# Performance work log

Measured on AMD Instinct MI355X. Metric: run time of the kernel, lower is better.

Reference implementation:

```python
import jax, jax.numpy as jnp
import numpy as np

NUM_USERS = 100000
NUM_ITEMS = 50000
NUM_HIDDEN = 64
NUM_BINS = 10
BATCH = 131072
N_QUAD = 64  # quadrature nodes in incomplete/complete beta
EPS = 1e-6


def _trapz0(y, dt):
    # trapezoidal rule along axis 0 with uniform spacing dt
    return (jnp.sum(y, axis=0) - 0.5 * (y[0] + y[-1])) * dt


def setup_inputs() -> dict:
    key = jax.random.key(0)
    ks = jax.random.split(key, 12)
    return {
        "uid_input": jax.random.randint(ks[0], (BATCH,), 0, NUM_USERS),
        "iid_input": jax.random.randint(ks[1], (BATCH,), 0, NUM_ITEMS),
        "uid_features": 0.1 * jax.random.normal(ks[2], (NUM_USERS, NUM_HIDDEN + 1), jnp.float32),
        "iid_features": 0.1 * jax.random.normal(ks[3], (NUM_ITEMS, NUM_HIDDEN + 1), jnp.float32),
        "uid_bin_terms": 0.1 * jax.random.normal(ks[4], (NUM_USERS, NUM_BINS), jnp.float32),
        "iid_bin_terms": 0.1 * jax.random.normal(ks[5], (NUM_ITEMS, NUM_BINS), jnp.float32),
        "uid_alpha_emb": 0.01 * jax.random.normal(ks[6], (NUM_USERS, 1), jnp.float32),
        "uid_beta_emb": 0.01 * jax.random.normal(ks[7], (NUM_USERS, 1), jnp.float32),
        "iid_alpha_emb": 0.01 * jax.random.normal(ks[8], (NUM_ITEMS, 1), jnp.float32),
        "iid_beta_emb": 0.01 * jax.random.normal(ks[9], (NUM_ITEMS, 1), jnp.float32),
        "global_bias": jnp.asarray(2.0, jnp.float32),
    }


def reference(uid_input, iid_input, uid_features, iid_features,
              uid_bin_terms, iid_bin_terms, uid_alpha_emb, uid_beta_emb,
              iid_alpha_emb, iid_beta_emb, global_bias):
    # embedding lookups (confidence features alias the regular features)
    uf = uid_features[uid_input]          # (B, H+1)
    vf = iid_features[iid_input]          # (B, H+1)
    u = uf[:, :-1]                        # (B, H)
    v = vf[:, :-1]

    # mu / upsilon (upsilon_layer_id == 2: |dot|)
    dot = jnp.sum(u * v, axis=-1, keepdims=True)                    # (B, 1)
    len_prod = (jnp.linalg.norm(u, axis=1, keepdims=True)
                * jnp.linalg.norm(v, axis=1, keepdims=True))
    mu = jnp.clip(0.5 + 0.5 * dot / jnp.maximum(len_prod, EPS), EPS, 1.0 - EPS)
    upsilon = jnp.maximum(jnp.abs(dot), EPS)

    # alpha / beta
    alpha = jnp.maximum(0.01, mu * upsilon)
    beta = jnp.maximum(0.01, upsilon - alpha)
    alpha = global_bias + alpha
    beta = global_bias + beta
    alpha = jnp.maximum(0.01, alpha + uid_alpha_emb[uid_input] + iid_alpha_emb[iid_input])  # (B,1)
    beta = jnp.maximum(0.01, beta + uid_beta_emb[uid_input] + iid_beta_emb[iid_input])      # (B,1)

    # per-pair bin edges via normalized exp + cumsum
    terms = jnp.exp(uid_bin_terms[uid_input] + iid_bin_terms[iid_input])  # (B, NUM_BINS)
    terms = terms / jnp.sum(terms, axis=-1, keepdims=True)
    edges = jnp.cumsum(terms, axis=-1)                                    # (B, NUM_BINS)

    # regularized incomplete beta at interior edges via trapezoidal quadrature
    x = edges[:, :-1]                                  # (B, NB-1)
    t = jnp.linspace(0.0, 1.0, N_QUAD, dtype=alpha.dtype)
    dt = t[1] - t[0]
    t3 = t[:, None, None]                              # (n, 1, 1)
    a3 = alpha[None, :, :]                             # (1, B, 1)
    b3 = beta[None, :, :]
    tx = t3 * x[None]                                  # (n, B, NB-1)
    integrand = (tx ** (a3 - 1.0)) * ((1.0 - tx) ** (b3 - 1.0))
    integrand = integrand * (t3 <= x[None]).astype(integrand.dtype)
    Bx_ab = _trapz0(integrand, dt)                     # (B, NB-1)

    # complete beta B(a, b)
    c_int = (t[None, :] ** (alpha - 1.0)) * ((1.0 - t[None, :]) ** (beta - 1.0))  # (B, n)
    B_ab = (jnp.sum(c_int, axis=-1) - 0.5 * (c_int[:, 0] + c_int[:, -1])) * dt    # (B,)

    cdf = Bx_ab / B_ab[:, None]                        # (B, NB-1)
    cdf = jnp.concatenate([cdf, jnp.ones_like(alpha)], axis=-1)  # (B, NB)
    mass = jnp.concatenate([cdf[:, :1], cdf[:, 1:] - cdf[:, :-1]], axis=-1)
    return mass
```

## Files before the change

### kernel.cpp

```cpp
#include <hip/hip_runtime.h>
#include <math.h>

#define BLOCK 256

__device__ __forceinline__ float exp2_fast(float x) {
#if __has_builtin(__builtin_amdgcn_exp2f)
    return __builtin_amdgcn_exp2f(x);
#else
    return __expf(x * 0.69314718055994531f);
#endif
}

__global__ __launch_bounds__(BLOCK) void lbd_kernel(
    const int* __restrict__ uid_in, const int* __restrict__ iid_in,
    const float* __restrict__ uf,  const float* __restrict__ vf,
    const float* __restrict__ ubt, const float* __restrict__ ibt,
    const float* __restrict__ uae, const float* __restrict__ ube,
    const float* __restrict__ iae, const float* __restrict__ ibe,
    const float* __restrict__ gbp, float* __restrict__ out, int B)
{
    const int tid = threadIdx.x;
    const int sub = tid & 15;
    const int s0  = blockIdx.x * (BLOCK / 16) + (tid >> 4);
    const bool valid = (s0 < B);
    const int s = valid ? s0 : (B - 1);

    const int u = uid_in[s];
    const int v = iid_in[s];

    const long long ub = (long long)u * 65;
    const long long vb = (long long)v * 65;
    float fu0 = uf[ub + sub],      fv0 = vf[vb + sub];
    float fu1 = uf[ub + 16 + sub], fv1 = vf[vb + 16 + sub];
    float fu2 = uf[ub + 32 + sub], fv2 = vf[vb + 32 + sub];
    float fu3 = uf[ub + 48 + sub], fv3 = vf[vb + 48 + sub];

    float dotp = fu0 * fv0 + fu1 * fv1 + fu2 * fv2 + fu3 * fv3;
    float sup  = fu0 * fu0 + fu1 * fu1 + fu2 * fu2 + fu3 * fu3;
    float svp  = fv0 * fv0 + fv1 * fv1 + fv2 * fv2 + fv3 * fv3;
#pragma unroll
    for (int d = 1; d < 16; d <<= 1) {
        dotp += __shfl_xor(dotp, d, 64);
        sup  += __shfl_xor(sup,  d, 64);
        svp  += __shfl_xor(svp,  d, 64);
    }

    const float gb = gbp[0];
    const float len_prod = sqrtf(sup) * sqrtf(svp);
    const float EPS = 1e-6f;
    const float HI  = (float)(1.0 - 1e-6);
    float mu = 0.5f + (0.5f * dotp) / fmaxf(len_prod, EPS);
    mu = fminf(fmaxf(mu, EPS), HI);
    const float ups = fmaxf(fabsf(dotp), EPS);
    const float al0 = fmaxf(0.01f, mu * ups);
    const float be0 = fmaxf(0.01f, ups - al0);
    const float alpha = fmaxf(0.01f, (gb + al0) + uae[u] + iae[v]);
    const float beta  = fmaxf(0.01f, (gb + be0) + ube[u] + ibe[v]);
    const float am1 = alpha - 1.0f;
    const float bm1 = beta  - 1.0f;

    const double STEP = 1.0 / 63.0;
    float xf_own = 0.f, lx_own = 0.f;
    int   im_own = 0;
    {
        double e = 0.0;
        if (sub < 10)
            e = exp((double)ubt[u * 10 + sub] + (double)ibt[v * 10 + sub]);
        double c = e;
#pragma unroll
        for (int d = 1; d < 16; d <<= 1) {
            double t = __shfl_up(c, d, 16);
            if (sub >= d) c += t;
        }
        const double ssum = __shfl(c, 9, 16);
        if (sub < 9) {
            const double x = c / ssum;
            int im = (int)(x * 63.0);
            if (im > 62) im = 62;
            while (im < 62 && (double)(im + 1) * STEP <= x) ++im;
            while (im >= 1 && (double)im * STEP > x) --im;
            im_own = im;
            xf_own = (float)x;
            lx_own = __log2f(xf_own);
        }
    }
    float xfj[9], alxj[9];
    int   imj[9], mbu[9];
#pragma unroll
    for (int j = 0; j < 9; ++j) {
        xfj[j]  = __shfl(xf_own, j, 16);
        alxj[j] = am1 * __shfl(lx_own, j, 16);
        imj[j]  = __shfl(im_own, j, 16);
        int mm  = imj[j];
        mm = max(mm, __shfl_xor(mm, 16, 64));
        mm = max(mm, __shfl_xor(mm, 32, 64));
        mbu[j] = __builtin_amdgcn_readfirstlane((mm >> 4) + 1);
    }

    float tfm[4], altm[4];
#pragma unroll
    for (int m = 0; m < 4; ++m) {
        const int i = m * 16 + sub;
        const float tf = (float)((double)i * STEP);
        tfm[m]  = tf;
        altm[m] = am1 * __log2f(tf);
    }

    float accD = 0.0f;
#pragma unroll
    for (int m = 0; m < 4; ++m) {
        const float l1 = __log2f(1.0f - tfm[m]);
        accD += exp2_fast(fmaf(bm1, l1, altm[m]));
    }

    float acc[9];
#pragma unroll
    for (int j = 0; j < 9; ++j) {
        const float xj  = xfj[j];
        const float axj = alxj[j];
        const int   imv = imj[j];
        float a = 0.0f;
        for (int m = 0; m < mbu[j]; ++m) {
            const int   i  = m * 16 + sub;
            const float w  = fmaf(-tfm[m], xj, 1.0f);
            const float e  = fmaf(bm1, __log2f(w), altm[m] + axj);
            const float y  = exp2_fast(e);
            const bool  ok = (unsigned)(i - 1) < (unsigned)imv;
            a += ok ? y : 0.0f;
        }
        acc[j] = a;
    }

#pragma unroll
    for (int d = 1; d < 16; d <<= 1) {
        accD += __shfl_xor(accD, d, 64);
#pragma unroll
        for (int j = 0; j < 9; ++j) acc[j] += __shfl_xor(acc[j], d, 64);
    }

    const float dtf = (float)(1.0 / 63.0);
    const float Bab = accD * dtf;
    const float rB  = 1.0f / Bab;
    float cdfv[9];
#pragma unroll
    for (int j = 0; j < 9; ++j) cdfv[j] = (acc[j] * dtf) * rB;

    float mo = cdfv[0];
#pragma unroll
    for (int j = 1; j < 9; ++j) mo = (sub == j) ? (cdfv[j] - cdfv[j - 1]) : mo;
    mo = (sub == 9) ? (1.0f - cdfv[8]) : mo;
    if (valid && sub < 10) out[(long long)s * 10 + sub] = mo;
}

extern "C" void kernel_launch(void* const* d_in, const int* in_sizes, int n_in,
                              void* d_out, int out_size, void* d_ws, size_t ws_size,
                              hipStream_t stream) {
    (void)n_in; (void)out_size; (void)d_ws; (void)ws_size;
    const int*   uid = (const int*)d_in[0];
    const int*   iid = (const int*)d_in[1];
    const float* uf  = (const float*)d_in[2];
    const float* vf  = (const float*)d_in[3];
    const float* ubt = (const float*)d_in[4];
    const float* ibt = (const float*)d_in[5];
    const float* uae = (const float*)d_in[6];
    const float* ube = (const float*)d_in[7];
    const float* iae = (const float*)d_in[8];
    const float* ibe = (const float*)d_in[9];
    const float* gb  = (const float*)d_in[10];
    float* out = (float*)d_out;
    const int B = in_sizes[0];
    const int samples_per_block = BLOCK / 16;
    const int grid = (B + samples_per_block - 1) / samples_per_block;
    hipLaunchKernelGGL(lbd_kernel, dim3(grid), dim3(BLOCK), 0, stream,
                       uid, iid, uf, vf, ubt, ibt, uae, ube, iae, ibe, gb, out, B);
}
```

Measured before the change: 140.1 us.

## Use shared quadrature table, fast f64 exp, and fully unrolled bin evaluation

Each block now precomputes the quadrature nodes and their log2 terms once into a shared-memory table, instead of every thread recomputing them. The double-precision libm exp is replaced by a custom polynomial exp. The per-bin loop with a variable trip count is turned into a fully unrolled m-by-j nest guarded by wave-uniform bounds, which exposes more ILP. This adds a __syncthreads and LDS reads, and the custom exp may differ slightly from libm in accuracy.

```diff
diff --git a/kernel.cpp b/kernel.cpp
--- a/kernel.cpp
+++ b/kernel.cpp
@@ -9,6 +9,31 @@
 #else
     return __expf(x * 0.69314718055994531f);
 #endif
+}
+
+__device__ __forceinline__ double exp_f64_fast(double x) {
+    const double L2E = 1.4426950408889634074;
+    const double LN2 = 0.69314718055994530942;
+    double z = x * L2E;
+    double n = rint(z);
+    double r = fma(x, L2E, -n);
+    double w = r * LN2;
+    double p = 2.08767569878680989792e-9;
+    p = fma(p, w, 2.50521083854417187751e-8);
+    p = fma(p, w, 2.75573192239858906526e-7);
+    p = fma(p, w, 2.75573192239858925110e-6);
+    p = fma(p, w, 2.48015873015873015873e-5);
+    p = fma(p, w, 1.98412698412698412698e-4);
+    p = fma(p, w, 1.38888888888888888889e-3);
+    p = fma(p, w, 8.33333333333333333333e-3);
+    p = fma(p, w, 4.16666666666666666667e-2);
+    p = fma(p, w, 1.66666666666666666667e-1);
+    p = fma(p, w, 0.5);
+    p = fma(p, w, 1.0);
+    p = fma(p, w, 1.0);
+    const int ni = (int)n;
+    const double sc = __longlong_as_double((long long)(1023 + ni) << 52);
+    return p * sc;
 }
 
 __global__ __launch_bounds__(BLOCK) void lbd_kernel(
@@ -19,7 +44,16 @@
     const float* __restrict__ iae, const float* __restrict__ ibe,
     const float* __restrict__ gbp, float* __restrict__ out, int B)
 {
+    __shared__ float4 s_tab[64];
     const int tid = threadIdx.x;
+    if (tid < 64) {
+        const double STEP0 = 1.0 / 63.0;
+        float tf = (float)((double)tid * STEP0);
+        if (tid == 63) tf = 1.0f;
+        s_tab[tid] = make_float4(tf, __log2f(tf), __log2f(1.0f - tf), 0.0f);
+    }
+    __syncthreads();
+
     const int sub = tid & 15;
     const int s0  = blockIdx.x * (BLOCK / 16) + (tid >> 4);
     const bool valid = (s0 < B);
@@ -65,7 +99,7 @@
     {
         double e = 0.0;
         if (sub < 10)
-            e = exp((double)ubt[u * 10 + sub] + (double)ibt[v * 10 + sub]);
+            e = exp_f64_fast((double)ubt[u * 10 + sub] + (double)ibt[v * 10 + sub]);
         double c = e;
 #pragma unroll
         for (int d = 1; d < 16; d <<= 1) {
@@ -85,7 +119,7 @@
         }
     }
     float xfj[9], alxj[9];
-    int   imj[9], mbu[9];
+    int   imj[9], imw[9];
 #pragma unroll
     for (int j = 0; j < 9; ++j) {
         xfj[j]  = __shfl(xf_own, j, 16);
@@ -94,42 +128,47 @@
         int mm  = imj[j];
         mm = max(mm, __shfl_xor(mm, 16, 64));
         mm = max(mm, __shfl_xor(mm, 32, 64));
-        mbu[j] = __builtin_amdgcn_readfirstlane((mm >> 4) + 1);
-    }
-
-    float tfm[4], altm[4];
+        imw[j] = __builtin_amdgcn_readfirstlane(mm);
+    }
+
+    float tfm[4], altm[4], l1m[4];
 #pragma unroll
     for (int m = 0; m < 4; ++m) {
-        const int i = m * 16 + sub;
-        const float tf = (float)((double)i * STEP);
-        tfm[m]  = tf;
-        altm[m] = am1 * __log2f(tf);
+        float4 e = s_tab[m * 16 + sub];
+        tfm[m]  = e.x;
+        altm[m] = am1 * e.y;
+        l1m[m]  = e.z;
     }
 
     float accD = 0.0f;
-#pragma unroll
-    for (int m = 0; m < 4; ++m) {
-        const float l1 = __log2f(1.0f - tfm[m]);
-        accD += exp2_fast(fmaf(bm1, l1, altm[m]));
-    }
-
     float acc[9];
 #pragma unroll
-    for (int j = 0; j < 9; ++j) {
-        const float xj  = xfj[j];
-        const float axj = alxj[j];
-        const int   imv = imj[j];
-        float a = 0.0f;
-        for (int m = 0; m < mbu[j]; ++m) {
-            const int   i  = m * 16 + sub;
-            const float w  = fmaf(-tfm[m], xj, 1.0f);
-            const float e  = fmaf(bm1, __log2f(w), altm[m] + axj);
-            const float y  = exp2_fast(e);
-            const bool  ok = (unsigned)(i - 1) < (unsigned)imv;
-            a += ok ? y : 0.0f;
+    for (int j = 0; j < 9; ++j) acc[j] = 0.0f;
+
+#define EVAL_MJ(m, j)                                                              \
+    do {                                                                           \
+        const float w_ = fmaf(-tfm[m], xfj[j], 1.0f);                              \
+        const float e_ = fmaf(bm1, __log2f(w_), altm[m] + alxj[j]);                \
+        const float y_ = exp2_fast(e_);                                            \
+        const int   i_ = (m) * 16 + sub;                                           \
+        acc[j] += ((unsigned)(i_ - 1) < (unsigned)imj[j]) ? y_ : 0.0f;             \
+    } while (0)
+
+#pragma unroll
+    for (int m = 0; m < 4; ++m)
+        accD += exp2_fast(fmaf(bm1, l1m[m], altm[m]));
+
+#pragma unroll
+    for (int j = 0; j < 9; ++j) EVAL_MJ(0, j);
+
+#pragma unroll
+    for (int m = 1; m < 4; ++m) {
+#pragma unroll
+        for (int j = 0; j < 9; ++j) {
+            if (imw[j] >= 16 * m) EVAL_MJ(m, j);
         }
-        acc[j] = a;
-    }
+    }
+#undef EVAL_MJ
 
 #pragma unroll
     for (int d = 1; d < 16; d <<= 1) {
```

New measurement: 137.8 us. About the same (-1.6%).
